# Performance work log

Measured on AMD Instinct MI355X. Metric: run time of the kernel, lower is better.

## Reference

```python
import jax, jax.numpy as jnp
import numpy as np

NEG_SLOPE = 0.2  # PyG GATConv leaky_relu slope


def _embed(feats, W1, b1, W2, b2, Wc, bc):
    # collapse_esm (two plain Linears, no activation) then linear_comb
    esm = feats[..., 24:] @ W1 + b1
    esm = esm @ W2 + b2
    x = jnp.concatenate([feats[..., :24], esm], axis=-1)
    return x @ Wc + bc


def _gat_conv(x, src, dst, n, W, a_src, a_dst, b, concat):
    # PyG GATConv: project, per-edge attention logits, softmax over incoming edges at dst,
    # weighted scatter-sum. Self loops already included in (src, dst).
    H, C = a_src.shape
    h = (x @ W).reshape(-1, H, C)                 # [N,H,C]
    s = (h * a_src).sum(-1)                       # [N,H]
    d = (h * a_dst).sum(-1)                       # [N,H]
    e = jax.nn.leaky_relu(s[src] + d[dst], NEG_SLOPE)  # [E,H]
    m = jax.ops.segment_max(e, dst, num_segments=n)
    e = jnp.exp(e - m[dst])
    z = jax.ops.segment_sum(e, dst, num_segments=n)
    alpha = e / z[dst]                            # [E,H]
    out = jax.ops.segment_sum(h[src] * alpha[:, :, None], dst, num_segments=n)  # [N,H,C]
    out = out.reshape(n, H * C) if concat else out.mean(axis=1)
    return out + b


def setup_inputs() -> dict:
    key = jax.random.key(0)
    ks = jax.random.split(key, 24)
    N, E, B, F = 100000, 3200000, 8, 50
    NF, M1, M2, M3, CH = 1304, 652, 326, 350, 32
    L, H, HID = 3, 8, 4
    f32 = jnp.float32
    inp = {
        "node_features": jax.random.normal(ks[0], (N, NF), f32),
        "edge_index": jax.random.randint(ks[1], (2, E), 0, N, dtype=jnp.int32),
        "edge_attr": jax.random.normal(ks[2], (E, 8), f32),
        "frag_emb": jax.random.normal(ks[3], (B, F, NF), f32),
        "W_esm1": jax.random.normal(ks[4], (NF - 24, M1), f32) / np.sqrt(NF - 24),
        "b_esm1": jnp.zeros((M1,), f32),
        "W_esm2": jax.random.normal(ks[5], (M1, M2), f32) / np.sqrt(M1),
        "b_esm2": jnp.zeros((M2,), f32),
        "W_comb": jax.random.normal(ks[6], (M3, CH), f32) / np.sqrt(M3),
        "b_comb": jnp.zeros((CH,), f32),
        "gat1_W": jax.random.normal(ks[7], (L, CH, H * HID), f32) / np.sqrt(CH),
        "gat1_asrc": jax.random.normal(ks[8], (L, H, HID), f32) * 0.1,
        "gat1_adst": jax.random.normal(ks[9], (L, H, HID), f32) * 0.1,
        "gat1_b": jnp.zeros((L, H * HID), f32),
        "gat2_W": jax.random.normal(ks[10], (L, H * HID, CH), f32) / np.sqrt(H * HID),
        "gat2_asrc": jax.random.normal(ks[11], (L, 1, CH), f32) * 0.1,
        "gat2_adst": jax.random.normal(ks[12], (L, 1, CH), f32) * 0.1,
        "gat2_b": jnp.zeros((L, CH), f32),
        "W_fin": jax.random.normal(ks[13], (CH, 1), f32) / np.sqrt(CH),
        "b_fin": jnp.zeros((1,), f32),
    }
    return inp


def reference(node_features, edge_index, edge_attr, frag_emb,
              W_esm1, b_esm1, W_esm2, b_esm2, W_comb, b_comb,
              gat1_W, gat1_asrc, gat1_adst, gat1_b,
              gat2_W, gat2_asrc, gat2_adst, gat2_b,
              W_fin, b_fin):
    N = node_features.shape[0]
    loop = jnp.arange(N, dtype=edge_index.dtype)
    src = jnp.concatenate([edge_index[0], loop])  # self loops (PyG default)
    dst = jnp.concatenate([edge_index[1], loop])

    x = _embed(node_features, W_esm1, b_esm1, W_esm2, b_esm2, W_comb, b_comb)  # [N,32]
    for i in range(gat1_W.shape[0]):
        x = _gat_conv(x, src, dst, N, gat1_W[i], gat1_asrc[i], gat1_adst[i], gat1_b[i], True)
        x = jax.nn.elu(x)
        x = _gat_conv(x, src, dst, N, gat2_W[i], gat2_asrc[i], gat2_adst[i], gat2_b[i], False)

    ys = _embed(frag_emb, W_esm1, b_esm1, W_esm2, b_esm2, W_comb, b_comb)  # [B,F,32]
    B, F, C = ys.shape
    xb = x.reshape(B, N // B, C)                      # equal-size graphs
    A = jax.nn.softmax(jnp.einsum('bnd,bfd->bnf', xb, ys), axis=-1)
    p = jnp.einsum('bnf,bfd->bnd', A, ys)             # [B,n,32]
    return jax.nn.sigmoid(p @ W_fin + b_fin).squeeze(-1)  # [B,n]
```

## Files before the change

kernel.cpp:

```cpp
#include <hip/hip_runtime.h>
#include <hip/hip_bf16.h>

#define NF 1304
#define M1 652
#define M2 326
#define CH 32
#define NHEAD1 8
#define HID1 4
#define NLAYER 3
#define FRAG 50
#define NBATCH 8
#define DPAD 32

static inline int ceil_div(int a, int b){ return (a + b - 1)/b; }

__device__ __forceinline__ unsigned short f2h(float f){
  _Float16 h = (_Float16)f;
  unsigned short u;
  __builtin_memcpy(&u, &h, 2);
  return u;
}
__device__ __forceinline__ float h2f(unsigned short u){
  _Float16 h;
  __builtin_memcpy(&h, &u, 2);
  return (float)h;
}

#define TM 64
#define TN 64
#define TKK 16
__global__ __launch_bounds__(256) void gemm_bias(
    const float* __restrict__ A, int lda,
    const float* __restrict__ B, int ldb,
    const float* __restrict__ bias,
    float* __restrict__ C, int ldc,
    int M, int N, int K, int acc)
{
  __shared__ float As[TKK][TM + 1];
  __shared__ float Bs[TKK][TN];
  int tid = threadIdx.x;
  int tx = tid & 15, ty = tid >> 4;
  int row0 = blockIdx.y * TM, col0 = blockIdx.x * TN;
  float c[4][4] = {};
  for (int k0 = 0; k0 < K; k0 += TKK) {
    #pragma unroll
    for (int p = 0; p < 4; ++p) {
      int r = (tid >> 4) + p * 16;
      int kk = tid & 15;
      int gr = row0 + r, gk = k0 + kk;
      float v = 0.f;
      if (gr < M && gk < K) v = A[(long long)gr * lda + gk];
      As[kk][r] = v;
    }
    #pragma unroll
    for (int p = 0; p < 4; ++p) {
      int kk = (tid >> 6) + p * 4;
      int cc = tid & 63;
      int gk = k0 + kk, gc = col0 + cc;
      float v = 0.f;
      if (gk < K && gc < N) v = B[(long long)gk * ldb + gc];
      Bs[kk][cc] = v;
    }
    __syncthreads();
    #pragma unroll
    for (int kk = 0; kk < TKK; ++kk) {
      float a[4], b[4];
      #pragma unroll
      for (int i = 0; i < 4; ++i) a[i] = As[kk][ty + 16 * i];
      #pragma unroll
      for (int j = 0; j < 4; ++j) b[j] = Bs[kk][tx + 16 * j];
      #pragma unroll
      for (int i = 0; i < 4; ++i)
        #pragma unroll
        for (int j = 0; j < 4; ++j)
          c[i][j] += a[i] * b[j];
    }
    __syncthreads();
  }
  #pragma unroll
  for (int i = 0; i < 4; ++i) {
    int gr = row0 + ty + 16 * i;
    if (gr >= M) continue;
    #pragma unroll
    for (int j = 0; j < 4; ++j) {
      int gc = col0 + tx + 16 * j;
      if (gc >= N) continue;
      float v = c[i][j];
      if (bias) v += bias[gc];
      if (acc) v += C[(long long)gr * ldc + gc];
      C[(long long)gr * ldc + gc] = v;
    }
  }
}

__global__ void fold_misc_kernel(const float* __restrict__ Wc, const float* __restrict__ T1,
                                 const float* __restrict__ b1, const float* __restrict__ b2,
                                 const float* __restrict__ bc,
                                 float* __restrict__ Wbig, float* __restrict__ bfold)
{
  int tid = threadIdx.x;
  for (int i = tid; i < 24 * CH; i += 256) Wbig[i] = Wc[i];
  if (tid < CH) {
    float v = bc[tid];
    for (int k = 0; k < M2; ++k) v += b2[k] * Wc[(24 + k) * CH + tid];
    for (int i = 0; i < M1; ++i) v += b1[i] * T1[i * CH + tid];
    bfold[tid] = v;
  }
}

#define EK 64
__device__ __forceinline__ void gemm_n32_body(
    const float* __restrict__ A, int M, int K,
    const float* __restrict__ W, const float* __restrict__ bias,
    float* __restrict__ C, int bid,
    float (*As)[65], float (*Ws)[32])
{
  int tid = threadIdx.x;
  int row0 = bid * 64;
  int tx = tid & 7, ty = tid >> 3;
  float c0[4] = {}, c1[4] = {};
  for (int k0 = 0; k0 < K; k0 += EK) {
    #pragma unroll
    for (int p = 0; p < 4; ++p) {
      int q = tid + p * 256;
      int r = q >> 4, c4 = (q & 15) * 4;
      int gr = row0 + r, gk = k0 + c4;
      float4 v = make_float4(0.f, 0.f, 0.f, 0.f);
      if (gr < M) {
        if (gk + 3 < K) v = *(const float4*)&A[(long long)gr * K + gk];
        else {
          float t[4] = {0.f, 0.f, 0.f, 0.f};
          for (int i = 0; i < 4; ++i) if (gk + i < K) t[i] = A[(long long)gr * K + gk + i];
          v = make_float4(t[0], t[1], t[2], t[3]);
        }
      }
      As[r][c4 + 0] = v.x; As[r][c4 + 1] = v.y; As[r][c4 + 2] = v.z; As[r][c4 + 3] = v.w;
    }
    #pragma unroll
    for (int p = 0; p < 2; ++p) {
      int q = tid + p * 256;
      int r = q >> 3, c4 = (q & 7) * 4;
      int gk = k0 + r;
      float4 v = make_float4(0.f, 0.f, 0.f, 0.f);
      if (gk < K) v = *(const float4*)&W[(long long)gk * 32 + c4];
      *(float4*)&Ws[r][c4] = v;
    }
    __syncthreads();
    #pragma unroll
    for (int kk = 0; kk < EK; ++kk) {
      float4 b = *(const float4*)&Ws[kk][tx * 4];
      float a0 = As[ty * 2][kk], a1 = As[ty * 2 + 1][kk];
      c0[0] += a0 * b.x; c0[1] += a0 * b.y; c0[2] += a0 * b.z; c0[3] += a0 * b.w;
      c1[0] += a1 * b.x; c1[1] += a1 * b.y; c1[2] += a1 * b.z; c1[3] += a1 * b.w;
    }
    __syncthreads();
  }
  float4 bb = *(const float4*)&bias[tx * 4];
  int gr0 = row0 + ty * 2;
  if (gr0 < M) {
    float4 v = make_float4(c0[0] + bb.x, c0[1] + bb.y, c0[2] + bb.z, c0[3] + bb.w);
    *(float4*)&C[(long long)gr0 * 32 + tx * 4] = v;
  }
  if (gr0 + 1 < M) {
    float4 v = make_float4(c1[0] + bb.x, c1[1] + bb.y, c1[2] + bb.z, c1[3] + bb.w);
    *(float4*)&C[(long long)(gr0 + 1) * 32 + tx * 4] = v;
  }
}

__global__ __launch_bounds__(256) void gemm_n32(
    const float* __restrict__ A, int M, int K,
    const float* __restrict__ W, const float* __restrict__ bias,
    float* __restrict__ C)
{
  __shared__ float As[64][65];
  __shared__ float Ws[EK][32];
  gemm_n32_body(A, M, K, W, bias, C, blockIdx.x, As, Ws);
}

__global__ __launch_bounds__(256) void fused_embed_rank(
    const float* __restrict__ A, int M, int K,
    const float* __restrict__ W, const float* __restrict__ bias,
    float* __restrict__ C, int nEmbed,
    const int* __restrict__ ei, int E,
    int* __restrict__ degp, int* __restrict__ rank)
{
  __shared__ float As[64][65];
  __shared__ float Ws[EK][32];
  int id = blockIdx.x;
  if (id % 9 == 0) {
    int eid = id / 9;
    if (eid >= nEmbed) return;
    gemm_n32_body(A, M, K, W, bias, C, eid, As, Ws);
  } else {
    int rid = id - id / 9 - 1;
    long long e = (long long)rid * 256 + threadIdx.x;
    if (e < E) rank[e] = atomicAdd(&degp[(long long)ei[E + e] * DPAD], 1);
  }
}

__global__ void zero_deg_kernel(int* __restrict__ degp, long long n)
{
  long long i = (long long)blockIdx.x * 256 + threadIdx.x;
  if (i < n) degp[i] = 0;
}
__global__ void partial_kernel(const int* __restrict__ degp, int N, int* __restrict__ partial)
{
  __shared__ int sd[256];
  int i = blockIdx.x * 256 + threadIdx.x;
  sd[threadIdx.x] = (i < N) ? degp[(long long)i * DPAD] : 0;
  __syncthreads();
  for (int off = 128; off > 0; off >>= 1) {
    if (threadIdx.x < off) sd[threadIdx.x] += sd[threadIdx.x + off];
    __syncthreads();
  }
  if (threadIdx.x == 0) partial[blockIdx.x] = sd[0];
}
__global__ void scanp_kernel(int* __restrict__ partial, int NB)
{
  __shared__ int sd[512];
  int t = threadIdx.x;
  int v = (t < NB) ? partial[t] : 0;
  sd[t] = v;
  __syncthreads();
  for (int off = 1; off < 512; off <<= 1) {
    int u = (t >= off) ? sd[t - off] : 0;
    __syncthreads();
    sd[t] += u;
    __syncthreads();
  }
  if (t < NB) partial[t] = sd[t] - v;
}
__global__ void scan_final_kernel(const int* __restrict__ degp, int N,
                                  const int* __restrict__ partial,
                                  int* __restrict__ rowptr)
{
  __shared__ int sd[256];
  int i = blockIdx.x * 256 + threadIdx.x;
  int t = threadIdx.x;
  int v = (i < N) ? degp[(long long)i * DPAD] : 0;
  sd[t] = v;
  __syncthreads();
  for (int off = 1; off < 256; off <<= 1) {
    int u = (t >= off) ? sd[t - off] : 0;
    __syncthreads();
    sd[t] += u;
    __syncthreads();
  }
  if (i < N) {
    int excl = partial[blockIdx.x] + sd[t] - v;
    rowptr[i] = excl;
    if (i == N - 1) rowptr[N] = excl + v;
  }
}
__global__ void scatter_plain_kernel(const int* __restrict__ ei, int E,
                                     const int* __restrict__ rowptr,
                                     const int* __restrict__ rank,
                                     int* __restrict__ csr)
{
  int e = blockIdx.x * 256 + threadIdx.x;
  if (e >= E) return;
  int dn = ei[E + e];
  csr[rowptr[dn] + rank[e]] = ei[e];
}

template<int H, int C>
__global__ __launch_bounds__(256) void proj_sd_kernel(
    const float* __restrict__ x, const float* __restrict__ W,
    const float* __restrict__ adst,
    unsigned* __restrict__ hp, float* __restrict__ dv, int N)
{
  __shared__ float Ws[CH][CH];
  __shared__ float al[CH];
  int tid = threadIdx.x;
  for (int i = tid; i < CH * CH; i += 256) Ws[i >> 5][i & 31] = W[i];
  if (tid < CH) al[tid] = adst[tid];
  __syncthreads();
  int n = blockIdx.x * 256 + tid;
  if (n >= N) return;
  float xr[CH];
  #pragma unroll
  for (int j = 0; j < CH / 4; ++j) {
    float4 v = *(const float4*)&x[(long long)n * CH + j * 4];
    xr[j * 4] = v.x; xr[j * 4 + 1] = v.y; xr[j * 4 + 2] = v.z; xr[j * 4 + 3] = v.w;
  }
  float hr[CH] = {};
  #pragma unroll
  for (int c = 0; c < CH; ++c) {
    float xc = xr[c];
    #pragma unroll
    for (int j4 = 0; j4 < CH / 4; ++j4) {
      float4 w = *(const float4*)&Ws[c][j4 * 4];
      hr[j4 * 4] += xc * w.x; hr[j4 * 4 + 1] += xc * w.y;
      hr[j4 * 4 + 2] += xc * w.z; hr[j4 * 4 + 3] += xc * w.w;
    }
  }
  unsigned pk[16];
  #pragma unroll
  for (int j = 0; j < 16; ++j)
    pk[j] = (unsigned)f2h(hr[2 * j]) | ((unsigned)f2h(hr[2 * j + 1]) << 16);
  uint4* hq = (uint4*)&hp[(long long)n * 16];
  #pragma unroll
  for (int j = 0; j < 4; ++j)
    hq[j] = make_uint4(pk[4 * j], pk[4 * j + 1], pk[4 * j + 2], pk[4 * j + 3]);
  #pragma unroll
  for (int hh = 0; hh < H; ++hh) {
    float dd = 0.f;
    #pragma unroll
    for (int c = 0; c < C; ++c) dd += hr[hh * C + c] * al[hh * C + c];
    dv[(long long)n * H + hh] = dd;
  }
}

template<int H, int C>
__global__ __launch_bounds__(256) void gat_gather_kernel(
    const int* __restrict__ rowptr, const int* __restrict__ csr,
    const unsigned* __restrict__ hp, const float* __restrict__ asrc,
    const float* __restrict__ dv, const float* __restrict__ bias,
    float* __restrict__ xout, int N, int do_elu)
{
  int wid = threadIdx.x >> 6;
  int lane = threadIdx.x & 63;
  int n = blockIdx.x * 4 + wid;
  if (n >= N) return;
  int cpair = lane & 15;
  int slot = lane >> 4;
  int ch = cpair * 2;
  int hh = (C == HID1) ? (cpair >> 1) : 0;
  float a0 = asrc[ch], a1 = asrc[ch + 1];
  float dn = dv[(long long)n * H + hh];

  auto sred = [&](float p) {
    p += __shfl_xor(p, 1, 64);
    if (C == CH) {
      p += __shfl_xor(p, 2, 64);
      p += __shfl_xor(p, 4, 64);
      p += __shfl_xor(p, 8, 64);
    }
    return p;
  };

  float acc0 = 0.f, acc1 = 0.f, z = 0.f;
  {
    unsigned u = hp[(long long)n * 16 + cpair];
    float h0 = h2f((unsigned short)(u & 0xffff));
    float h1 = h2f((unsigned short)(u >> 16));
    float s = sred(h0 * a0 + h1 * a1);
    if (slot == 0) {
      float lg = s + dn;
      lg = lg > 0.f ? lg : 0.2f * lg;
      float w = expf(lg);
      z = w; acc0 = w * h0; acc1 = w * h1;
    }
  }
  int start = rowptr[n], end = rowptr[n + 1];
  for (int base = start; base < end; base += 64) {
    int m = end - base; if (m > 64) m = 64;
    int idx = (base + lane < end) ? csr[base + lane] : 0;
    int k = slot;
    for (; k + 12 < m; k += 16) {
      int si0 = __shfl(idx, k, 64);
      int si1 = __shfl(idx, k + 4, 64);
      int si2 = __shfl(idx, k + 8, 64);
      int si3 = __shfl(idx, k + 12, 64);
      unsigned u0 = hp[(long long)si0 * 16 + cpair];
      unsigned u1 = hp[(long long)si1 * 16 + cpair];
      unsigned u2 = hp[(long long)si2 * 16 + cpair];
      unsigned u3 = hp[(long long)si3 * 16 + cpair];
      float h00 = h2f((unsigned short)(u0 & 0xffff)), h01 = h2f((unsigned short)(u0 >> 16));
      float h10 = h2f((unsigned short)(u1 & 0xffff)), h11 = h2f((unsigned short)(u1 >> 16));
      float h20 = h2f((unsigned short)(u2 & 0xffff)), h21 = h2f((unsigned short)(u2 >> 16));
      float h30 = h2f((unsigned short)(u3 & 0xffff)), h31 = h2f((unsigned short)(u3 >> 16));
      float s0 = sred(h00 * a0 + h01 * a1);
      float s1 = sred(h10 * a0 + h11 * a1);
      float s2 = sred(h20 * a0 + h21 * a1);
      float s3 = sred(h30 * a0 + h31 * a1);
      float lg0 = s0 + dn; lg0 = lg0 > 0.f ? lg0 : 0.2f * lg0;
      float lg1 = s1 + dn; lg1 = lg1 > 0.f ? lg1 : 0.2f * lg1;
      float lg2 = s2 + dn; lg2 = lg2 > 0.f ? lg2 : 0.2f * lg2;
      float lg3 = s3 + dn; lg3 = lg3 > 0.f ? lg3 : 0.2f * lg3;
      float w0 = expf(lg0), w1 = expf(lg1), w2 = expf(lg2), w3 = expf(lg3);
      z += (w0 + w1) + (w2 + w3);
      acc0 += w0 * h00 + w1 * h10 + w2 * h20 + w3 * h30;
      acc1 += w0 * h01 + w1 * h11 + w2 * h21 + w3 * h31;
    }
    for (; k < m; k += 4) {
      int si0 = __shfl(idx, k, 64);
      unsigned u0 = hp[(long long)si0 * 16 + cpair];
      float h00 = h2f((unsigned short)(u0 & 0xffff)), h01 = h2f((unsigned short)(u0 >> 16));
      float s0 = sred(h00 * a0 + h01 * a1);
      float lg0 = s0 + dn; lg0 = lg0 > 0.f ? lg0 : 0.2f * lg0;
      float w0 = expf(lg0);
      z += w0;
      acc0 += w0 * h00;
      acc1 += w0 * h01;
    }
  }
  acc0 += __shfl_xor(acc0, 16, 64); acc0 += __shfl_xor(acc0, 32, 64);
  acc1 += __shfl_xor(acc1, 16, 64); acc1 += __shfl_xor(acc1, 32, 64);
  z    += __shfl_xor(z, 16, 64);    z    += __shfl_xor(z, 32, 64);
  if (slot == 0) {
    float v0 = acc0 / z + bias[ch];
    float v1 = acc1 / z + bias[ch + 1];
    if (do_elu) {
      v0 = v0 > 0.f ? v0 : (expf(v0) - 1.f);
      v1 = v1 > 0.f ? v1 : (expf(v1) - 1.f);
    }
    *(float2*)&xout[(long long)n * 32 + ch] = make_float2(v0, v1);
  }
}

__global__ __launch_bounds__(256) void pool_kernel(
    const float* __restrict__ x, const float* __restrict__ ys,
    const float* __restrict__ Wfin, const float* __restrict__ bfin,
    float* __restrict__ out, int NB)
{
  __shared__ float ysl[FRAG][CH];
  __shared__ float tl[FRAG];
  int b = blockIdx.y;
  int tid = threadIdx.x;
  for (int idx = tid; idx < FRAG * CH; idx += 256)
    ysl[idx >> 5][idx & 31] = ys[(long long)b * FRAG * CH + idx];
  __syncthreads();
  if (tid < FRAG) {
    float t = 0.f;
    #pragma unroll
    for (int dd = 0; dd < CH; ++dd) t += ysl[tid][dd] * Wfin[dd];
    tl[tid] = t;
  }
  __syncthreads();
  int n = blockIdx.x * 256 + tid;
  if (n >= NB) return;
  const float* xr = x + ((long long)b * NB + n) * CH;
  float xreg[CH];
  #pragma unroll
  for (int dd = 0; dd < CH; ++dd) xreg[dd] = xr[dd];
  float mx = -1e30f;
  for (int f = 0; f < FRAG; ++f) {
    float l = 0.f;
    #pragma unroll
    for (int dd = 0; dd < CH; ++dd) l += xreg[dd] * ysl[f][dd];
    mx = fmaxf(mx, l);
  }
  float se = 0.f, sw = 0.f;
  for (int f = 0; f < FRAG; ++f) {
    float l = 0.f;
    #pragma unroll
    for (int dd = 0; dd < CH; ++dd) l += xreg[dd] * ysl[f][dd];
    float e = expf(l - mx);
    se += e; sw += e * tl[f];
  }
  float logit = sw / se + bfin[0];
  out[(long long)b * NB + n] = 1.f / (1.f + expf(-logit));
}

extern "C" void kernel_launch(void* const* d_in, const int* in_sizes, int n_in,
                              void* d_out, int out_size, void* d_ws, size_t ws_size,
                              hipStream_t stream)
{
  const float* feats = (const float*)d_in[0];
  const int*   ei    = (const int*)d_in[1];
  const float* frag  = (const float*)d_in[3];
  const float* W1    = (const float*)d_in[4];
  const float* b1    = (const float*)d_in[5];
  const float* W2    = (const float*)d_in[6];
  const float* b2    = (const float*)d_in[7];
  const float* Wc    = (const float*)d_in[8];
  const float* bc    = (const float*)d_in[9];
  const float* g1W   = (const float*)d_in[10];
  const float* g1as  = (const float*)d_in[11];
  const float* g1ad  = (const float*)d_in[12];
  const float* g1b   = (const float*)d_in[13];
  const float* g2W   = (const float*)d_in[14];
  const float* g2as  = (const float*)d_in[15];
  const float* g2ad  = (const float*)d_in[16];
  const float* g2b   = (const float*)d_in[17];
  const float* Wfin  = (const float*)d_in[18];
  const float* bfin  = (const float*)d_in[19];

  const int N  = in_sizes[0] / NF;
  const int E  = in_sizes[1] / 2;
  const int BF = in_sizes[3] / NF;
  const int NB = N / NBATCH;

  char* ws = (char*)d_ws;
  size_t off = 0;
  auto walloc = [&](size_t bytes) -> void* {
    void* p = ws + off;
    off += (bytes + 255) & ~(size_t)255;
    return p;
  };
  float*    T1     = (float*)walloc((size_t)M1 * CH * 4);
  float*    Wbig   = (float*)walloc((size_t)NF * CH * 4);
  float*    bfold  = (float*)walloc((size_t)CH * 4);
  float*    x0     = (float*)walloc((size_t)N * CH * 4);
  float*    x1     = (float*)walloc((size_t)N * CH * 4);
  unsigned* hbuf   = (unsigned*)walloc((size_t)N * 16 * 4);
  float*    dbuf   = (float*)walloc((size_t)N * NHEAD1 * 4);
  float*    ysb    = (float*)walloc((size_t)BF * CH * 4);
  int*      degp   = (int*)walloc((size_t)N * DPAD * 4);
  int*      rowptr = (int*)walloc((size_t)(N + 1) * 4);
  int*      rank   = (int*)walloc((size_t)E * 4);
  int*      part   = (int*)walloc((size_t)512 * 4);
  int*      csr    = (int*)walloc((size_t)E * 4);
  (void)ws_size; (void)n_in; (void)out_size;

  {
    dim3 g1(1, ceil_div(M1, TM));
    gemm_bias<<<g1, 256, 0, stream>>>(W2, M2, Wc + 24 * CH, CH, nullptr, T1, CH,
                                      M1, CH, M2, 0);
    dim3 g2(1, ceil_div(NF - 24, TM));
    gemm_bias<<<g2, 256, 0, stream>>>(W1, M1, T1, CH, nullptr, Wbig + 24 * CH, CH,
                                      NF - 24, CH, M1, 0);
    fold_misc_kernel<<<1, 256, 0, stream>>>(Wc, T1, b1, b2, bc, Wbig, bfold);
  }

  {
    long long npad = (long long)N * DPAD;
    zero_deg_kernel<<<(int)((npad + 255) / 256), 256, 0, stream>>>(degp, npad);
    int nEmbed = ceil_div(N, 64);
    int rankB = ceil_div(E, 256);
    int G = 9 * nEmbed;
    int embedSlots = (G + 8) / 9;
    int rankSlots = G - embedSlots;
    if (rankSlots < rankB) G += (rankB - rankSlots) * 9 / 8 + 9;
    fused_embed_rank<<<G, 256, 0, stream>>>(feats, N, NF, Wbig, bfold, x0,
                                            nEmbed, ei, E, degp, rank);
  }

  {
    int nb = ceil_div(N, 256);
    partial_kernel<<<nb, 256, 0, stream>>>(degp, N, part);
    scanp_kernel<<<1, 512, 0, stream>>>(part, nb);
    scan_final_kernel<<<nb, 256, 0, stream>>>(degp, N, part, rowptr);
    scatter_plain_kernel<<<ceil_div(E, 256), 256, 0, stream>>>(ei, E, rowptr, rank, csr);
  }

  gemm_n32<<<ceil_div(BF, 64), 256, 0, stream>>>(frag, BF, NF, Wbig, bfold, ysb);

  auto conv = [&](const float* xin, float* xout, const float* W, const float* as_,
                  const float* ad_, const float* bias, int H, int do_elu) {
    if (H == NHEAD1) {
      proj_sd_kernel<NHEAD1, HID1><<<ceil_div(N, 256), 256, 0, stream>>>(
          xin, W, ad_, hbuf, dbuf, N);
      gat_gather_kernel<NHEAD1, HID1><<<ceil_div(N, 4), 256, 0, stream>>>(
          rowptr, csr, hbuf, as_, dbuf, bias, xout, N, do_elu);
    } else {
      proj_sd_kernel<1, CH><<<ceil_div(N, 256), 256, 0, stream>>>(
          xin, W, ad_, hbuf, dbuf, N);
      gat_gather_kernel<1, CH><<<ceil_div(N, 4), 256, 0, stream>>>(
          rowptr, csr, hbuf, as_, dbuf, bias, xout, N, do_elu);
    }
  };

  for (int l = 0; l < NLAYER; ++l) {
    conv(x0, x1, g1W + l * CH * CH, g1as + l * NHEAD1 * HID1, g1ad + l * NHEAD1 * HID1,
         g1b + l * CH, NHEAD1, 1);
    conv(x1, x0, g2W + l * CH * CH, g2as + l * CH, g2ad + l * CH,
         g2b + l * CH, 1, 0);
  }

  pool_kernel<<<dim3(ceil_div(NB, 256), NBATCH), 256, 0, stream>>>(
      x0, ysb, Wfin, bfin, (float*)d_out, NB);
}
```

Measured before the change: 1.331 ms.

## Unfuse embed/rank kernel and batch 16 independent neighbor loads per slot in gather

Splits the combined embedding-GEMM/edge-rank kernel into separate rank and GEMM launches. Rewrites the GAT gather inner loop so each slot reads a contiguous run of 16 CSR indices and issues 16 independent feature loads before computing attention weights. The intent is more loads in flight per thread. The cost is masked-out work for low-degree nodes and losing the overlap between the GEMM and the atomics.

```diff
diff --git a/kernel.cpp b/kernel.cpp
--- a/kernel.cpp
+++ b/kernel.cpp
@@ -109,14 +109,15 @@
 }
 
 #define EK 64
-__device__ __forceinline__ void gemm_n32_body(
+__global__ __launch_bounds__(256) void gemm_n32(
     const float* __restrict__ A, int M, int K,
     const float* __restrict__ W, const float* __restrict__ bias,
-    float* __restrict__ C, int bid,
-    float (*As)[65], float (*Ws)[32])
-{
+    float* __restrict__ C)
+{
+  __shared__ float As[64][65];
+  __shared__ float Ws[EK][32];
   int tid = threadIdx.x;
-  int row0 = bid * 64;
+  int row0 = blockIdx.x * 64;
   int tx = tid & 7, ty = tid >> 3;
   float c0[4] = {}, c1[4] = {};
   for (int k0 = 0; k0 < K; k0 += EK) {
@@ -167,41 +168,16 @@
   }
 }
 
-__global__ __launch_bounds__(256) void gemm_n32(
-    const float* __restrict__ A, int M, int K,
-    const float* __restrict__ W, const float* __restrict__ bias,
-    float* __restrict__ C)
-{
-  __shared__ float As[64][65];
-  __shared__ float Ws[EK][32];
-  gemm_n32_body(A, M, K, W, bias, C, blockIdx.x, As, Ws);
-}
-
-__global__ __launch_bounds__(256) void fused_embed_rank(
-    const float* __restrict__ A, int M, int K,
-    const float* __restrict__ W, const float* __restrict__ bias,
-    float* __restrict__ C, int nEmbed,
-    const int* __restrict__ ei, int E,
-    int* __restrict__ degp, int* __restrict__ rank)
-{
-  __shared__ float As[64][65];
-  __shared__ float Ws[EK][32];
-  int id = blockIdx.x;
-  if (id % 9 == 0) {
-    int eid = id / 9;
-    if (eid >= nEmbed) return;
-    gemm_n32_body(A, M, K, W, bias, C, eid, As, Ws);
-  } else {
-    int rid = id - id / 9 - 1;
-    long long e = (long long)rid * 256 + threadIdx.x;
-    if (e < E) rank[e] = atomicAdd(&degp[(long long)ei[E + e] * DPAD], 1);
-  }
-}
-
 __global__ void zero_deg_kernel(int* __restrict__ degp, long long n)
 {
   long long i = (long long)blockIdx.x * 256 + threadIdx.x;
   if (i < n) degp[i] = 0;
+}
+__global__ void rank_kernel(const int* __restrict__ ei, int E,
+                            int* __restrict__ degp, int* __restrict__ rank)
+{
+  int e = blockIdx.x * 256 + threadIdx.x;
+  if (e < E) rank[e] = atomicAdd(&degp[(long long)ei[E + e] * DPAD], 1);
 }
 __global__ void partial_kernel(const int* __restrict__ degp, int N, int* __restrict__ partial)
 {
@@ -354,45 +330,28 @@
   }
   int start = rowptr[n], end = rowptr[n + 1];
   for (int base = start; base < end; base += 64) {
-    int m = end - base; if (m > 64) m = 64;
-    int idx = (base + lane < end) ? csr[base + lane] : 0;
-    int k = slot;
-    for (; k + 12 < m; k += 16) {
-      int si0 = __shfl(idx, k, 64);
-      int si1 = __shfl(idx, k + 4, 64);
-      int si2 = __shfl(idx, k + 8, 64);
-      int si3 = __shfl(idx, k + 12, 64);
-      unsigned u0 = hp[(long long)si0 * 16 + cpair];
-      unsigned u1 = hp[(long long)si1 * 16 + cpair];
-      unsigned u2 = hp[(long long)si2 * 16 + cpair];
-      unsigned u3 = hp[(long long)si3 * 16 + cpair];
-      float h00 = h2f((unsigned short)(u0 & 0xffff)), h01 = h2f((unsigned short)(u0 >> 16));
-      float h10 = h2f((unsigned short)(u1 & 0xffff)), h11 = h2f((unsigned short)(u1 >> 16));
-      float h20 = h2f((unsigned short)(u2 & 0xffff)), h21 = h2f((unsigned short)(u2 >> 16));
-      float h30 = h2f((unsigned short)(u3 & 0xffff)), h31 = h2f((unsigned short)(u3 >> 16));
-      float s0 = sred(h00 * a0 + h01 * a1);
-      float s1 = sred(h10 * a0 + h11 * a1);
-      float s2 = sred(h20 * a0 + h21 * a1);
-      float s3 = sred(h30 * a0 + h31 * a1);
-      float lg0 = s0 + dn; lg0 = lg0 > 0.f ? lg0 : 0.2f * lg0;
-      float lg1 = s1 + dn; lg1 = lg1 > 0.f ? lg1 : 0.2f * lg1;
-      float lg2 = s2 + dn; lg2 = lg2 > 0.f ? lg2 : 0.2f * lg2;
-      float lg3 = s3 + dn; lg3 = lg3 > 0.f ? lg3 : 0.2f * lg3;
-      float w0 = expf(lg0), w1 = expf(lg1), w2 = expf(lg2), w3 = expf(lg3);
-      z += (w0 + w1) + (w2 + w3);
-      acc0 += w0 * h00 + w1 * h10 + w2 * h20 + w3 * h30;
-      acc1 += w0 * h01 + w1 * h11 + w2 * h21 + w3 * h31;
-    }
-    for (; k < m; k += 4) {
-      int si0 = __shfl(idx, k, 64);
-      unsigned u0 = hp[(long long)si0 * 16 + cpair];
-      float h00 = h2f((unsigned short)(u0 & 0xffff)), h01 = h2f((unsigned short)(u0 >> 16));
-      float s0 = sred(h00 * a0 + h01 * a1);
-      float lg0 = s0 + dn; lg0 = lg0 > 0.f ? lg0 : 0.2f * lg0;
-      float w0 = expf(lg0);
-      z += w0;
-      acc0 += w0 * h00;
-      acc1 += w0 * h01;
+    int b0 = base + slot * 16;
+    int idx[16];
+    #pragma unroll
+    for (int t = 0; t < 16; ++t) {
+      int p = b0 + t;
+      idx[t] = (p < end) ? csr[p] : -1;
+    }
+    unsigned uu[16];
+    #pragma unroll
+    for (int t = 0; t < 16; ++t)
+      uu[t] = (idx[t] >= 0) ? hp[(long long)idx[t] * 16 + cpair] : 0u;
+    #pragma unroll
+    for (int t = 0; t < 16; ++t) {
+      float h0 = h2f((unsigned short)(uu[t] & 0xffff));
+      float h1 = h2f((unsigned short)(uu[t] >> 16));
+      float s = sred(h0 * a0 + h1 * a1);
+      float lg = s + dn;
+      lg = lg > 0.f ? lg : 0.2f * lg;
+      float w = (idx[t] >= 0) ? expf(lg) : 0.f;
+      z += w;
+      acc0 += w * h0;
+      acc1 += w * h1;
     }
   }
   acc0 += __shfl_xor(acc0, 16, 64); acc0 += __shfl_xor(acc0, 32, 64);
@@ -516,25 +475,16 @@
 
   {
     long long npad = (long long)N * DPAD;
+    int nb = ceil_div(N, 256);
     zero_deg_kernel<<<(int)((npad + 255) / 256), 256, 0, stream>>>(degp, npad);
-    int nEmbed = ceil_div(N, 64);
-    int rankB = ceil_div(E, 256);
-    int G = 9 * nEmbed;
-    int embedSlots = (G + 8) / 9;
-    int rankSlots = G - embedSlots;
-    if (rankSlots < rankB) G += (rankB - rankSlots) * 9 / 8 + 9;
-    fused_embed_rank<<<G, 256, 0, stream>>>(feats, N, NF, Wbig, bfold, x0,
-                                            nEmbed, ei, E, degp, rank);
-  }
-
-  {
-    int nb = ceil_div(N, 256);
+    rank_kernel<<<ceil_div(E, 256), 256, 0, stream>>>(ei, E, degp, rank);
     partial_kernel<<<nb, 256, 0, stream>>>(degp, N, part);
     scanp_kernel<<<1, 512, 0, stream>>>(part, nb);
     scan_final_kernel<<<nb, 256, 0, stream>>>(degp, N, part, rowptr);
     scatter_plain_kernel<<<ceil_div(E, 256), 256, 0, stream>>>(ei, E, rowptr, rank, csr);
   }
 
+  gemm_n32<<<ceil_div(N, 64), 256, 0, stream>>>(feats, N, NF, Wbig, bfold, x0);
   gemm_n32<<<ceil_div(BF, 64), 256, 0, stream>>>(frag, BF, NF, Wbig, bfold, ysb);
 
   auto conv = [&](const float* xin, float* xout, const float* W, const float* as_,
```

Result: slower. 1.497 ms (+12.5%).
